# Performance work log

Measured on AMD Instinct MI355X. Metric: run time of the kernel, lower is better.

## Reference

```python
import jax, jax.numpy as jnp
import numpy as np

MARGIN = 1.0      # init kwarg
EPS = 1e-6        # torch pairwise_distance eps (added to the difference)
NUM_IDS = 64      # instance IDs in [0, 64); 0 is background, skipped


def setup_inputs() -> dict:
    key = jax.random.key(0)
    k1, k2 = jax.random.split(key)
    features = jax.random.normal(k1, (2, 256, 512, 512), dtype=jnp.float32)
    instance_mask = jax.random.randint(k2, (512, 512), 0, NUM_IDS, dtype=jnp.int32)
    return {"features": features, "instance_mask": instance_mask}


def _dist(a, b):
    # torch TripletMarginLoss uses pairwise_distance: ||a - b + eps||_2
    d = a - b + EPS
    return jnp.sqrt(jnp.sum(d * d))


def _loss(features, instance_mask):
    B, C, H, W = features.shape
    flat_mask = instance_mask.reshape(-1)                 # (HW,)
    feats = features.reshape(B * C, H * W)                # (BC, HW): a pixel -> (1, B*C) embedding
    base_key = jax.random.key(42)
    ids = jnp.arange(1, NUM_IDS, dtype=jnp.int32)         # skip background id 0

    def per_inst(inst):
        m = flat_mask == inst                             # (HW,) bool, row-major order
        cnt = m.sum()
        first = jnp.argmax(m)                             # first pixel of instance
        second = jnp.argmax(m.at[first].set(False))       # second pixel of instance
        neg = ~m                                          # torch: instance_mask != inst (incl. 0 and 255)
        ncnt = neg.sum()
        # random negative pixel: r-th True in neg
        r = jax.random.randint(jax.random.fold_in(base_key, inst), (), 0,
                               jnp.maximum(ncnt, 1))
        cum = jnp.cumsum(neg.astype(jnp.int32))
        nidx = jnp.argmax(cum >= r + 1)
        a = feats[:, first]
        p = feats[:, second]
        n = feats[:, nidx]
        l = jnp.maximum(_dist(a, p) - _dist(a, n) + MARGIN, 0.0)
        valid = (cnt >= 2) & (ncnt > 0)
        return jnp.where(valid, l, 0.0), valid.astype(jnp.float32)

    losses, valids = jax.vmap(per_inst)(ids)
    count = valids.sum()
    return jnp.where(count > 0, losses.sum() / jnp.maximum(count, 1.0),
                     jnp.float32(0.0))


def reference(features, instance_mask):
    return _loss(features, instance_mask)
```

## Files before the change

### kernel.cpp

```cpp
#include <hip/hip_runtime.h>

#define HW_N     (512 * 512)
#define ROWS     512
#define NINST    63
#define NCHUNK   256
#define CHUNK    1024

#define WS_HIST  1024

__device__ __forceinline__ unsigned rotl32(unsigned v, int r) {
    return (v << r) | (v >> (32 - r));
}

__device__ void threefry2x32(unsigned k0, unsigned k1,
                             unsigned x0, unsigned x1,
                             unsigned* o0, unsigned* o1) {
    const unsigned ks0 = k0, ks1 = k1;
    const unsigned ks2 = k0 ^ k1 ^ 0x1BD11BDAu;
    x0 += ks0; x1 += ks1;
    x0 += x1; x1 = rotl32(x1, 13); x1 ^= x0;
    x0 += x1; x1 = rotl32(x1, 15); x1 ^= x0;
    x0 += x1; x1 = rotl32(x1, 26); x1 ^= x0;
    x0 += x1; x1 = rotl32(x1,  6); x1 ^= x0;
    x0 += ks1; x1 += ks2 + 1u;
    x0 += x1; x1 = rotl32(x1, 17); x1 ^= x0;
    x0 += x1; x1 = rotl32(x1, 29); x1 ^= x0;
    x0 += x1; x1 = rotl32(x1, 16); x1 ^= x0;
    x0 += x1; x1 = rotl32(x1, 24); x1 ^= x0;
    x0 += ks2; x1 += ks0 + 2u;
    x0 += x1; x1 = rotl32(x1, 13); x1 ^= x0;
    x0 += x1; x1 = rotl32(x1, 15); x1 ^= x0;
    x0 += x1; x1 = rotl32(x1, 26); x1 ^= x0;
    x0 += x1; x1 = rotl32(x1,  6); x1 ^= x0;
    x0 += ks0; x1 += ks1 + 3u;
    x0 += x1; x1 = rotl32(x1, 17); x1 ^= x0;
    x0 += x1; x1 = rotl32(x1, 29); x1 ^= x0;
    x0 += x1; x1 = rotl32(x1, 16); x1 ^= x0;
    x0 += x1; x1 = rotl32(x1, 24); x1 ^= x0;
    x0 += ks1; x1 += ks2 + 4u;
    x0 += x1; x1 = rotl32(x1, 13); x1 ^= x0;
    x0 += x1; x1 = rotl32(x1, 15); x1 ^= x0;
    x0 += x1; x1 = rotl32(x1, 26); x1 ^= x0;
    x0 += x1; x1 = rotl32(x1,  6); x1 ^= x0;
    x0 += ks2; x1 += ks0 + 5u;
    *o0 = x0; *o1 = x1;
}

__device__ int block_scan_incl(int x, int tid, int* wsum ) {
    const int lane = tid & 63, wid = tid >> 6;
    for (int off = 1; off < 64; off <<= 1) {
        int y = __shfl_up(x, off, 64);
        if (lane >= off) x += y;
    }
    if (lane == 63) wsum[wid] = x;
    __syncthreads();
    int add = 0;
    for (int w = 0; w < wid; w++) add += wsum[w];
    x += add;
    __syncthreads();
    return x;
}

__global__ void icl_hist_kernel(const int* __restrict__ mask, int* __restrict__ ws) {
    const int c = blockIdx.x;
    const int tid = threadIdx.x;
    __shared__ int h[64];
    if (tid < 64) h[tid] = 0;
    __syncthreads();
    const int4 v = ((const int4*)(mask + c * CHUNK))[tid];
    if ((unsigned)v.x < 64u) atomicAdd(&h[v.x], 1);
    if ((unsigned)v.y < 64u) atomicAdd(&h[v.y], 1);
    if ((unsigned)v.z < 64u) atomicAdd(&h[v.z], 1);
    if ((unsigned)v.w < 64u) atomicAdd(&h[v.w], 1);
    __syncthreads();
    if (tid < 64) ws[WS_HIST + c * 64 + tid] = h[tid];
}

__global__ void icl_inst_kernel(const int* __restrict__ mask,
                                const float* __restrict__ feats,
                                int* __restrict__ ws,
                                float* __restrict__ wsf) {
    const int inst = blockIdx.x + 1;
    const int tid = threadIdx.x;

    __shared__ int wsum[4];
    __shared__ int s_cnt;
    __shared__ unsigned s_r;
    __shared__ int s_ch[3], s_k[3], s_idx[3];
    __shared__ float sred[8];

    if (tid == 0) {
        s_ch[0] = s_ch[1] = s_ch[2] = -1;
        s_k[0] = 1; s_k[1] = 0; s_k[2] = 0;
        s_idx[0] = s_idx[1] = s_idx[2] = 0;
    }

    const int h = ws[WS_HIST + tid * 64 + inst];
    const int incl = block_scan_incl(h, tid, wsum);
    const int excl = incl - h;
    if (tid == 255) s_cnt = incl;
    if (excl == 0 && incl >= 1) s_ch[0] = tid;
    if (excl < 2 && incl >= 2) { s_ch[1] = tid; s_k[1] = 2 - excl; }
    __syncthreads();

    const int cnt = s_cnt;
    const int ncnt = HW_N - cnt;
    if (tid == 0) {
        unsigned span = (unsigned)((ncnt > 1) ? ncnt : 1);
        unsigned f0, f1, k1a, k1b, k2a, k2b, h0, h1, l0, l1;
        threefry2x32(0u, 42u, 0u, (unsigned)inst, &f0, &f1);
        threefry2x32(f0, f1, 0u, 0u, &k1a, &k1b);
        threefry2x32(f0, f1, 0u, 1u, &k2a, &k2b);
        threefry2x32(k1a, k1b, 0u, 0u, &h0, &h1);
        threefry2x32(k2a, k2b, 0u, 0u, &l0, &l1);
        const unsigned hi = h0 ^ h1, lo = l0 ^ l1;
        unsigned mult = 65536u % span;
        mult = (mult * mult) % span;
        s_r = ((hi % span) * mult + (lo % span)) % span;
    }
    __syncthreads();

    const long long target = (long long)s_r + 1;
    const long long negincl = (long long)(tid + 1) * CHUNK - incl;
    const long long negexcl = (long long)tid * CHUNK - excl;
    if (negexcl < target && target <= negincl) {
        s_ch[2] = tid; s_k[2] = (int)(target - negexcl);
    }
    __syncthreads();

    for (int t = 0; t < 3; t++) {
        const int chunk = s_ch[t];
        if (chunk >= 0) {
            const int k = s_k[t];
            const int4 v = ((const int4*)(mask + chunk * CHUNK))[tid];
            int f0 = (v.x == inst), f1 = (v.y == inst), f2 = (v.z == inst), f3 = (v.w == inst);
            if (t == 2) { f0 = !f0; f1 = !f1; f2 = !f2; f3 = !f3; }
            const int mycnt = f0 + f1 + f2 + f3;
            const int minc = block_scan_incl(mycnt, tid, wsum);
            const int mexc = minc - mycnt;
            if (mexc < k && k <= minc) {
                int need = k - mexc, j = 3;
                if (f0 && --need == 0) j = 0;
                else if (f1 && --need == 0) j = 1;
                else if (f2 && --need == 0) j = 2;
                s_idx[t] = chunk * CHUNK + tid * 4 + j;
            }
        }
        __syncthreads();
    }

    const int valid = (cnt >= 2 && ncnt > 0) ? 1 : 0;
    const int iF = s_idx[0], iS = s_idx[1], iN = s_idx[2];
    float sap = 0.f, san = 0.f;
    if (valid) {
        for (int row = tid; row < ROWS; row += 256) {
            const size_t off = (size_t)row * HW_N;
            const float a = feats[off + iF];
            const float p = feats[off + iS];
            const float n = feats[off + iN];
            const float dp = a - p + 1e-6f;
            const float dn = a - n + 1e-6f;
            sap += dp * dp;
            san += dn * dn;
        }
    }
    for (int off = 32; off > 0; off >>= 1) {
        sap += __shfl_down(sap, off, 64);
        san += __shfl_down(san, off, 64);
    }
    const int lane = tid & 63, wid = tid >> 6;
    if (lane == 0) { sred[wid] = sap; sred[4 + wid] = san; }
    __syncthreads();
    if (tid == 0) {
        float t1 = sred[0] + sred[1] + sred[2] + sred[3];
        float t2 = sred[4] + sred[5] + sred[6] + sred[7];
        const float l = fmaxf(sqrtf(t1) - sqrtf(t2) + 1.0f, 0.0f);
        wsf[inst] = valid ? l : 0.0f;
        ws[320 + inst] = valid;
    }
}

__global__ void icl_final_kernel(const int* __restrict__ ws,
                                 const float* __restrict__ wsf,
                                 float* __restrict__ out) {
    if (threadIdx.x == 0 && blockIdx.x == 0) {
        float s = 0.f, cntv = 0.f;
        for (int i = 1; i <= NINST; i++) {
            s += wsf[i];
            cntv += (float)ws[320 + i];
        }
        out[0] = (cntv > 0.f) ? (s / fmaxf(cntv, 1.0f)) : 0.0f;
    }
}

extern "C" void kernel_launch(void* const* d_in, const int* in_sizes, int n_in,
                              void* d_out, int out_size, void* d_ws, size_t ws_size,
                              hipStream_t stream) {
    const float* feats = (const float*)d_in[0];
    const int*   mask  = (const int*)d_in[1];
    float* out = (float*)d_out;
    int*   wsi = (int*)d_ws;
    float* wsf = ((float*)d_ws) + 384;

    icl_hist_kernel <<<NCHUNK, 256, 0, stream>>>(mask, wsi);
    icl_inst_kernel <<<NINST, 256, 0, stream>>>(mask, feats, wsi, wsf);
    icl_final_kernel<<<1, 64, 0, stream>>>(wsi, wsf, out);
}
```

Measured before the change: 19.20 us.

## Fuse final reduction into instance kernel via last-block atomic counter

```diff
diff --git a/kernel.cpp b/kernel.cpp
--- a/kernel.cpp
+++ b/kernel.cpp
@@ -6,6 +6,7 @@
 #define NCHUNK   256
 #define CHUNK    1024
 
+#define WS_CTR   448
 #define WS_HIST  1024
 
 __device__ __forceinline__ unsigned rotl32(unsigned v, int r) {
@@ -66,6 +67,7 @@
     const int tid = threadIdx.x;
     __shared__ int h[64];
     if (tid < 64) h[tid] = 0;
+    if (c == 0 && tid == 0) ws[WS_CTR] = 0;
     __syncthreads();
     const int4 v = ((const int4*)(mask + c * CHUNK))[tid];
     if ((unsigned)v.x < 64u) atomicAdd(&h[v.x], 1);
@@ -73,13 +75,14 @@
     if ((unsigned)v.z < 64u) atomicAdd(&h[v.z], 1);
     if ((unsigned)v.w < 64u) atomicAdd(&h[v.w], 1);
     __syncthreads();
-    if (tid < 64) ws[WS_HIST + c * 64 + tid] = h[tid];
+    if (tid < 64) ws[WS_HIST + tid * NCHUNK + c] = h[tid];
 }
 
 __global__ void icl_inst_kernel(const int* __restrict__ mask,
                                 const float* __restrict__ feats,
                                 int* __restrict__ ws,
-                                float* __restrict__ wsf) {
+                                float* __restrict__ wsf,
+                                float* __restrict__ out) {
     const int inst = blockIdx.x + 1;
     const int tid = threadIdx.x;
 
@@ -88,6 +91,7 @@
     __shared__ unsigned s_r;
     __shared__ int s_ch[3], s_k[3], s_idx[3];
     __shared__ float sred[8];
+    __shared__ int s_last;
 
     if (tid == 0) {
         s_ch[0] = s_ch[1] = s_ch[2] = -1;
@@ -95,9 +99,9 @@
         s_idx[0] = s_idx[1] = s_idx[2] = 0;
     }
 
-    const int h = ws[WS_HIST + tid * 64 + inst];
-    const int incl = block_scan_incl(h, tid, wsum);
-    const int excl = incl - h;
+    const int hh = ws[WS_HIST + inst * NCHUNK + tid];
+    const int incl = block_scan_incl(hh, tid, wsum);
+    const int excl = incl - hh;
     if (tid == 255) s_cnt = incl;
     if (excl == 0 && incl >= 1) s_ch[0] = tid;
     if (excl < 2 && incl >= 2) { s_ch[1] = tid; s_k[1] = 2 - excl; }
@@ -128,11 +132,19 @@
     }
     __syncthreads();
 
+    int4 vt[3];
+    #pragma unroll
+    for (int t = 0; t < 3; t++) {
+        const int chunk = s_ch[t];
+        if (chunk >= 0) vt[t] = ((const int4*)(mask + chunk * CHUNK))[tid];
+    }
+
+    #pragma unroll
     for (int t = 0; t < 3; t++) {
         const int chunk = s_ch[t];
         if (chunk >= 0) {
             const int k = s_k[t];
-            const int4 v = ((const int4*)(mask + chunk * CHUNK))[tid];
+            const int4 v = vt[t];
             int f0 = (v.x == inst), f1 = (v.y == inst), f2 = (v.z == inst), f3 = (v.w == inst);
             if (t == 2) { f0 = !f0; f1 = !f1; f2 = !f2; f3 = !f3; }
             const int mycnt = f0 + f1 + f2 + f3;
@@ -177,19 +189,24 @@
         const float l = fmaxf(sqrtf(t1) - sqrtf(t2) + 1.0f, 0.0f);
         wsf[inst] = valid ? l : 0.0f;
         ws[320 + inst] = valid;
-    }
-}
-
-__global__ void icl_final_kernel(const int* __restrict__ ws,
-                                 const float* __restrict__ wsf,
-                                 float* __restrict__ out) {
-    if (threadIdx.x == 0 && blockIdx.x == 0) {
-        float s = 0.f, cntv = 0.f;
-        for (int i = 1; i <= NINST; i++) {
-            s += wsf[i];
-            cntv += (float)ws[320 + i];
-        }
-        out[0] = (cntv > 0.f) ? (s / fmaxf(cntv, 1.0f)) : 0.0f;
+        __threadfence();
+        const unsigned old = atomicAdd((unsigned*)&ws[WS_CTR], 1u);
+        s_last = (old == NINST - 1);
+    }
+    __syncthreads();
+
+    if (s_last && tid < 64) {
+        __threadfence();
+        float l = 0.f, v = 0.f;
+        if (tid >= 1 && tid <= NINST) {
+            l = __hip_atomic_load(&wsf[tid], __ATOMIC_RELAXED, __HIP_MEMORY_SCOPE_AGENT);
+            v = (float)__hip_atomic_load(&ws[320 + tid], __ATOMIC_RELAXED, __HIP_MEMORY_SCOPE_AGENT);
+        }
+        for (int off = 32; off > 0; off >>= 1) {
+            l += __shfl_down(l, off, 64);
+            v += __shfl_down(v, off, 64);
+        }
+        if (tid == 0) out[0] = (v > 0.f) ? (l / fmaxf(v, 1.0f)) : 0.0f;
     }
 }
 
@@ -203,6 +220,5 @@
     float* wsf = ((float*)d_ws) + 384;
 
     icl_hist_kernel <<<NCHUNK, 256, 0, stream>>>(mask, wsi);
-    icl_inst_kernel <<<NINST, 256, 0, stream>>>(mask, feats, wsi, wsf);
-    icl_final_kernel<<<1, 64, 0, stream>>>(wsi, wsf, out);
-}
+    icl_inst_kernel <<<NINST, 256, 0, stream>>>(mask, feats, wsi, wsf, out);
+}
```

New measurement: 19.25 us. No clear change (+0.3%).
